# Performance work log

Hardware: AMD Instinct MI355X
Metric: run time of the kernel (lower is better)

The kernel has to match this reference:

```python
import jax, jax.numpy as jnp
import numpy as np

GROUPS = 1  # module-level groups arg


def adaptive_avg_pool(x, out_size):
    # Equal-tile average pool (exact match to torch AdaptiveAvgPool2d when H,W divisible by out_size)
    b, c, h, w = x.shape
    fh, fw = h // out_size, w // out_size
    return x.reshape(b, c, out_size, fh, out_size, fw).mean(axis=(3, 5))


def setup_inputs() -> dict:
    key = jax.random.key(0)
    k1, k2, k3, k4 = jax.random.split(key, 4)
    x = jax.random.normal(k1, (64, 128, 80, 80), jnp.float32)
    weight = jax.random.normal(k2, (128, 128, 3, 3), jnp.float32) * 0.05   # static conv weight [out, icg, k, k]
    w_att = jax.random.normal(k3, (16384, 1, 3, 3), jnp.float32) * 0.05    # conv_att weight (groups=icg=128)
    b_att = jax.random.normal(k4, (16384,), jnp.float32) * 0.05            # conv_att bias
    return {"x": x, "weight": weight, "w_att": w_att, "b_att": b_att}


def reference(x, weight, w_att, b_att):
    b, cin, h, w = x.shape
    out_ch, icg, k, _ = weight.shape  # icg = in_channels // groups
    pad = 1

    # attention branch: adaptive avg pool to (k+2), grouped 3x3 VALID conv -> [b, out*icg, k, k]
    avg = adaptive_avg_pool(x, k + 2)
    att = jax.lax.conv_general_dilated(avg, w_att, (1, 1), "VALID",
                                       feature_group_count=icg)
    att = jax.nn.sigmoid(att + b_att[None, :, None, None])
    att = att.reshape(b, out_ch, icg, k, k)

    # per-sample dynamic kernels
    dyn_w = weight[None] * att                    # [b, out, icg, k, k]

    # batch-grouped conv: fold batch into channels, groups = b * GROUPS
    xg = x.reshape(1, b * cin, h, w)
    wg = dyn_w.reshape(b * out_ch, icg, k, k)
    out = jax.lax.conv_general_dilated(xg, wg, (1, 1), [(pad, pad), (pad, pad)],
                                       feature_group_count=b * GROUPS)
    return out.reshape(b, out_ch, out.shape[-2], out.shape[-1])
```

## Files before the change

### kernel.cpp

```cpp
#include <hip/hip_runtime.h>

typedef __bf16 bf16;
typedef __bf16 bf16x8 __attribute__((ext_vector_type(8)));
typedef float f32x16 __attribute__((ext_vector_type(16)));

#define NB 64
#define NC 128
#define HW 80

#define XT_BYTES  110166016L
#define W2_BYTES  18874368L
#define AVG_BYTES 819200L
#define WS_NEEDED (XT_BYTES + W2_BYTES + AVG_BYTES)

__device__ __forceinline__ void async16(const void* g, void* l) {
    __builtin_amdgcn_global_load_lds((const __attribute__((address_space(1))) void*)g,
                                     (__attribute__((address_space(3))) void*)l, 16, 0, 0);
}

__global__ void zero_halo(bf16* __restrict__ xT) {
    int b = blockIdx.x;
    long base = (long)b * 82 * 82 * 128;
    uint4 z = make_uint4(0u, 0u, 0u, 0u);
    for (int k = threadIdx.x; k < 5184; k += 256) {
        long off;
        if (k < 1312) {
            off = (long)k * 8;
        } else if (k < 2624) {
            off = (long)81 * 82 * 128 + (long)(k - 1312) * 8;
        } else {
            int r = k - 2624;
            int Y = (r >> 5) + 1;
            int side = (r >> 4) & 1;
            int cq = r & 15;
            off = ((long)Y * 82 + side * 81) * 128 + cq * 8;
        }
        *reinterpret_cast<uint4*>(xT + base + off) = z;
    }
}

__global__ void transpose_kernel(const float* __restrict__ x, bf16* __restrict__ xT) {
    __shared__ __align__(16) bf16 tile[64 * 68];
    int b = blockIdx.z, icb = blockIdx.y, pxb = blockIdx.x;
    int t = threadIdx.x;
    int pl = t & 63;
    int ig = t >> 6;
    const float* src = x + ((long)(b * 128 + icb * 64) * 6400) + pxb * 64;
    #pragma unroll
    for (int it = 0; it < 16; ++it) {
        int ic = ig * 16 + it;
        float v = src[(long)ic * 6400 + pl];
        tile[pl * 68 + ic] = (bf16)v;
    }
    __syncthreads();
    #pragma unroll
    for (int it = 0; it < 4; ++it) {
        int idx = it * 256 + t;
        int pxl = idx >> 4;
        int icq = idx & 15;
        int px = pxb * 64 + pxl;
        int Y = px / 80 + 1, X = px % 80 + 1;
        uint2 v = *reinterpret_cast<const uint2*>(&tile[pxl * 68 + icq * 4]);
        *reinterpret_cast<uint2*>(&xT[(((long)b * 82 + Y) * 82 + X) * 128 + icb * 64 + icq * 4]) = v;
    }
}

__global__ void pool_kernel(const bf16* __restrict__ xT, float* __restrict__ avg) {
    __shared__ float part[256][8];
    int bid = blockIdx.x;
    int j = bid % 5; int t2 = bid / 5; int i = t2 % 5; int b = t2 / 5;
    int t = threadIdx.x;
    int pxg = t >> 4, cc = t & 15;
    const bf16* src = xT + (((long)b * 82 + 1 + i * 16) * 82 + 1 + j * 16 + pxg) * 128 + cc * 8;
    float s[8];
    #pragma unroll
    for (int e = 0; e < 8; ++e) s[e] = 0.f;
    #pragma unroll
    for (int dy = 0; dy < 16; ++dy) {
        bf16x8 v = *reinterpret_cast<const bf16x8*>(src + (long)dy * 82 * 128);
        #pragma unroll
        for (int e = 0; e < 8; ++e) s[e] += (float)v[e];
    }
    #pragma unroll
    for (int e = 0; e < 8; ++e) part[t][e] = s[e];
    __syncthreads();
    if (t < 128) {
        int cc2 = t >> 3, e = t & 7;
        float sum = 0.f;
        #pragma unroll
        for (int g = 0; g < 16; ++g) sum += part[g * 16 + cc2][e];
        avg[(((long)b * 128 + cc2 * 8 + e) * 5 + i) * 5 + j] = sum * (1.0f / 256.0f);
    }
}

__global__ void att_kernel(const float* __restrict__ avg, const float* __restrict__ weight,
                           const float* __restrict__ w_att, const float* __restrict__ b_att,
                           bf16* __restrict__ W2) {
    __shared__ float sa[25];
    int b = blockIdx.x >> 7, och = blockIdx.x & 127;
    int ic = threadIdx.x;
    if (ic < 25) sa[ic] = avg[(long)blockIdx.x * 25 + ic];
    __syncthreads();
    int o = och * 128 + ic;
    float wa[9];
    #pragma unroll
    for (int j = 0; j < 9; ++j) wa[j] = w_att[(long)o * 9 + j];
    float bias = b_att[o];
    const float* wst = weight + (long)o * 9;
    #pragma unroll
    for (int kh = 0; kh < 3; ++kh) {
        #pragma unroll
        for (int kw = 0; kw < 3; ++kw) {
            float z = bias;
            #pragma unroll
            for (int di = 0; di < 3; ++di)
                #pragma unroll
                for (int dj = 0; dj < 3; ++dj)
                    z += sa[(kh + di) * 5 + (kw + dj)] * wa[di * 3 + dj];
            float s = 1.0f / (1.0f + __expf(-z));
            float dw = wst[kh * 3 + kw] * s;
            int p = kh * 3 + kw;
            W2[(((long)b * 9 + p) * 128 + och) * 128 + ic] = (bf16)dw;
        }
    }
}

__global__ __launch_bounds__(256, 2)
void conv_gemm(const bf16* __restrict__ xT, const bf16* __restrict__ W2,
               float* __restrict__ out) {
    __shared__ __align__(16) bf16 Xs[180 * 128];
    __shared__ __align__(16) bf16 Ws[2][128 * 64];
    int b = blockIdx.z;
    int px0 = blockIdx.x * 16;
    int py0 = blockIdx.y * 8;
    int t = threadIdx.x;
    int wave = t >> 6, lane = t & 63;
    int l31 = lane & 31, hl = lane >> 5;
    int ow = (wave >> 1) * 64;
    int nw = (wave & 1) * 64;

    {
        const bf16* xsrc = xT + (((long)b * 82 + py0) * 82 + px0) * 128;
        for (int cidx = wave; cidx < 45; cidx += 4) {
            int idx0 = cidx << 6;
            int idx = idx0 + lane;
            int pf = idx >> 4, icb = idx & 15;
            int r = pf / 18, cx = pf - r * 18;
            async16(xsrc + ((long)r * 82 + cx) * 128 + ((icb ^ (pf & 7)) << 3),
                    &Xs[idx0 * 8]);
        }
        const bf16* wsrc = W2 + (long)b * 9 * 16384;
        #pragma unroll
        for (int it = 0; it < 4; ++it) {
            int idx0 = it * 256 + (wave << 6);
            int idx = idx0 + lane;
            int och = idx >> 3, icb = idx & 7;
            async16(wsrc + och * 128 + ((icb ^ (och & 7)) << 3), &Ws[0][idx0 * 8]);
        }
    }
    asm volatile("s_waitcnt vmcnt(0)" ::: "memory");
    __builtin_amdgcn_s_barrier();
    asm volatile("" ::: "memory");

    f32x16 acc[2][2];
    #pragma unroll
    for (int mi = 0; mi < 2; ++mi)
        #pragma unroll
        for (int ni = 0; ni < 2; ++ni)
            #pragma unroll
            for (int r = 0; r < 16; ++r) acc[mi][ni][r] = 0.f;

    int aRow0 = (ow + l31) * 64;
    int sA = l31 & 7;
    int pfb = ((nw + l31) >> 4) * 18 + ((nw + l31) & 15);

    #pragma unroll
    for (int tt = 0; tt < 18; ++tt) {
        int p = tt >> 1, h = tt & 1;
        int kh = p / 3, kw = p - kh * 3;
        if (tt < 17) {
            int p2 = (tt + 1) >> 1, h2 = (tt + 1) & 1;
            const bf16* wsrc = W2 + ((long)b * 9 + p2) * 16384 + h2 * 64;
            bf16* ldst = &Ws[(tt + 1) & 1][0];
            #pragma unroll
            for (int it = 0; it < 4; ++it) {
                int idx0 = it * 256 + (wave << 6);
                int idx = idx0 + lane;
                int och = idx >> 3, icb = idx & 7;
                async16(wsrc + och * 128 + ((icb ^ (och & 7)) << 3), ldst + idx0 * 8);
            }
        }
        const bf16* Wb = &Ws[tt & 1][0];
        __builtin_amdgcn_s_setprio(1);
        #pragma unroll
        for (int ks = 0; ks < 4; ++ks) {
            int icb = ks * 2 + hl;
            bf16x8 a0 = *reinterpret_cast<const bf16x8*>(Wb + aRow0 + ((icb ^ sA) << 3));
            bf16x8 a1 = *reinterpret_cast<const bf16x8*>(Wb + aRow0 + 2048 + ((icb ^ sA) << 3));
            int icbx = h * 8 + icb;
            int pf0 = pfb + kh * 18 + kw;
            int pf1 = pf0 + 36;
            bf16x8 b0 = *reinterpret_cast<const bf16x8*>(&Xs[pf0 * 128 + ((icbx ^ (pf0 & 7)) << 3)]);
            bf16x8 b1 = *reinterpret_cast<const bf16x8*>(&Xs[pf1 * 128 + ((icbx ^ (pf1 & 7)) << 3)]);
            acc[0][0] = __builtin_amdgcn_mfma_f32_32x32x16_bf16(a0, b0, acc[0][0], 0, 0, 0);
            acc[0][1] = __builtin_amdgcn_mfma_f32_32x32x16_bf16(a0, b1, acc[0][1], 0, 0, 0);
            acc[1][0] = __builtin_amdgcn_mfma_f32_32x32x16_bf16(a1, b0, acc[1][0], 0, 0, 0);
            acc[1][1] = __builtin_amdgcn_mfma_f32_32x32x16_bf16(a1, b1, acc[1][1], 0, 0, 0);
        }
        __builtin_amdgcn_s_setprio(0);
        __builtin_amdgcn_sched_barrier(0);
        asm volatile("s_waitcnt vmcnt(0)" ::: "memory");
        __builtin_amdgcn_s_barrier();
        asm volatile("" ::: "memory");
    }

    #pragma unroll
    for (int mi = 0; mi < 2; ++mi) {
        #pragma unroll
        for (int ni = 0; ni < 2; ++ni) {
            int n = nw + ni * 32 + l31;
            int oy = py0 + (n >> 4), ox = px0 + (n & 15);
            float* ob = out + ((long)(b * 128 + ow + mi * 32 + 4 * hl) * 80 + oy) * 80 + ox;
            #pragma unroll
            for (int reg = 0; reg < 16; ++reg) {
                int row = (reg & 3) + 8 * (reg >> 2);
                ob[(long)row * 6400] = acc[mi][ni][reg];
            }
        }
    }
}

extern "C" void kernel_launch(void* const* d_in, const int* in_sizes, int n_in,
                              void* d_out, int out_size, void* d_ws, size_t ws_size,
                              hipStream_t stream) {
    const float* x      = (const float*)d_in[0];
    const float* weight = (const float*)d_in[1];
    const float* w_att  = (const float*)d_in[2];
    const float* b_att  = (const float*)d_in[3];
    float* out = (float*)d_out;

    if (ws_size < (size_t)WS_NEEDED) return;

    char* ws = (char*)d_ws;
    bf16* xT  = (bf16*)ws;
    bf16* W2  = (bf16*)(ws + XT_BYTES);
    float* avg = (float*)(ws + XT_BYTES + W2_BYTES);

    zero_halo<<<64, 256, 0, stream>>>(xT);
    transpose_kernel<<<dim3(100, 2, 64), 256, 0, stream>>>(x, xT);
    pool_kernel<<<1600, 256, 0, stream>>>(xT, avg);
    att_kernel<<<8192, 128, 0, stream>>>(avg, weight, w_att, b_att, W2);
    conv_gemm<<<dim3(5, 10, 64), 256, 0, stream>>>(xT, W2, out);
}
```

Before: 521.5 us.

## Fuse pool+attention, merge halo zeroing, read conv weights directly from global

Folds halo zeroing into the transpose kernel and merges pooling and attention into one kernel, reducing launches and the avg round-trip. The dynamic weights are written in an MFMA-fragment-friendly layout so the conv kernel loads A operands straight from global memory instead of double-buffering them through LDS with per-step barriers. This frees LDS so occupancy can rise to 3 blocks per CU. The trade-off is exposed global load latency in the MFMA loop and a low-parallelism pool_att kernel with serialized barriers.

```diff
diff --git a/kernel.cpp b/kernel.cpp
--- a/kernel.cpp
+++ b/kernel.cpp
@@ -1,48 +1,47 @@
 #include <hip/hip_runtime.h>
 
 typedef __bf16 bf16;
+typedef __bf16 bf16x2 __attribute__((ext_vector_type(2)));
 typedef __bf16 bf16x8 __attribute__((ext_vector_type(8)));
 typedef float f32x16 __attribute__((ext_vector_type(16)));
 
-#define NB 64
-#define NC 128
-#define HW 80
-
 #define XT_BYTES  110166016L
 #define W2_BYTES  18874368L
-#define AVG_BYTES 819200L
-#define WS_NEEDED (XT_BYTES + W2_BYTES + AVG_BYTES)
+#define WS_NEEDED (XT_BYTES + W2_BYTES)
 
 __device__ __forceinline__ void async16(const void* g, void* l) {
     __builtin_amdgcn_global_load_lds((const __attribute__((address_space(1))) void*)g,
                                      (__attribute__((address_space(3))) void*)l, 16, 0, 0);
-}
-
-__global__ void zero_halo(bf16* __restrict__ xT) {
-    int b = blockIdx.x;
-    long base = (long)b * 82 * 82 * 128;
-    uint4 z = make_uint4(0u, 0u, 0u, 0u);
-    for (int k = threadIdx.x; k < 5184; k += 256) {
-        long off;
-        if (k < 1312) {
-            off = (long)k * 8;
-        } else if (k < 2624) {
-            off = (long)81 * 82 * 128 + (long)(k - 1312) * 8;
-        } else {
-            int r = k - 2624;
-            int Y = (r >> 5) + 1;
-            int side = (r >> 4) & 1;
-            int cq = r & 15;
-            off = ((long)Y * 82 + side * 81) * 128 + cq * 8;
-        }
-        *reinterpret_cast<uint4*>(xT + base + off) = z;
-    }
 }
 
 __global__ void transpose_kernel(const float* __restrict__ x, bf16* __restrict__ xT) {
     __shared__ __align__(16) bf16 tile[64 * 68];
     int b = blockIdx.z, icb = blockIdx.y, pxb = blockIdx.x;
     int t = threadIdx.x;
+
+    {
+        int bid2 = blockIdx.y * 100 + blockIdx.x;
+        if (t < 26) {
+            int k = bid2 * 26 + t;
+            if (k < 5184) {
+                long off;
+                if (k < 1312) {
+                    off = (long)k * 8;
+                } else if (k < 2624) {
+                    off = (long)81 * 82 * 128 + (long)(k - 1312) * 8;
+                } else {
+                    int r = k - 2624;
+                    int Y = (r >> 5) + 1;
+                    int side = (r >> 4) & 1;
+                    int cq = r & 15;
+                    off = ((long)Y * 82 + side * 81) * 128 + cq * 8;
+                }
+                *reinterpret_cast<uint4*>(xT + (long)b * 82 * 82 * 128 + off) =
+                    make_uint4(0u, 0u, 0u, 0u);
+            }
+        }
+    }
+
     int pl = t & 63;
     int ig = t >> 6;
     const float* src = x + ((long)(b * 128 + icb * 64) * 6400) + pxb * 64;
@@ -65,71 +64,74 @@
     }
 }
 
-__global__ void pool_kernel(const bf16* __restrict__ xT, float* __restrict__ avg) {
-    __shared__ float part[256][8];
-    int bid = blockIdx.x;
-    int j = bid % 5; int t2 = bid / 5; int i = t2 % 5; int b = t2 / 5;
+__global__ void pool_att(const bf16* __restrict__ xT, const float* __restrict__ weight,
+                         const float* __restrict__ w_att, const float* __restrict__ b_att,
+                         bf16* __restrict__ W2k) {
+    __shared__ float part[16][16][2];
+    __shared__ float avgs[32][25];
+    int b = blockIdx.x >> 2, cg = blockIdx.x & 3;
     int t = threadIdx.x;
-    int pxg = t >> 4, cc = t & 15;
-    const bf16* src = xT + (((long)b * 82 + 1 + i * 16) * 82 + 1 + j * 16 + pxg) * 128 + cc * 8;
-    float s[8];
-    #pragma unroll
-    for (int e = 0; e < 8; ++e) s[e] = 0.f;
-    #pragma unroll
-    for (int dy = 0; dy < 16; ++dy) {
-        bf16x8 v = *reinterpret_cast<const bf16x8*>(src + (long)dy * 82 * 128);
-        #pragma unroll
-        for (int e = 0; e < 8; ++e) s[e] += (float)v[e];
-    }
-    #pragma unroll
-    for (int e = 0; e < 8; ++e) part[t][e] = s[e];
-    __syncthreads();
-    if (t < 128) {
-        int cc2 = t >> 3, e = t & 7;
-        float sum = 0.f;
-        #pragma unroll
-        for (int g = 0; g < 16; ++g) sum += part[g * 16 + cc2][e];
-        avg[(((long)b * 128 + cc2 * 8 + e) * 5 + i) * 5 + j] = sum * (1.0f / 256.0f);
-    }
-}
-
-__global__ void att_kernel(const float* __restrict__ avg, const float* __restrict__ weight,
-                           const float* __restrict__ w_att, const float* __restrict__ b_att,
-                           bf16* __restrict__ W2) {
-    __shared__ float sa[25];
-    int b = blockIdx.x >> 7, och = blockIdx.x & 127;
-    int ic = threadIdx.x;
-    if (ic < 25) sa[ic] = avg[(long)blockIdx.x * 25 + ic];
-    __syncthreads();
-    int o = och * 128 + ic;
-    float wa[9];
-    #pragma unroll
-    for (int j = 0; j < 9; ++j) wa[j] = w_att[(long)o * 9 + j];
-    float bias = b_att[o];
-    const float* wst = weight + (long)o * 9;
-    #pragma unroll
-    for (int kh = 0; kh < 3; ++kh) {
-        #pragma unroll
-        for (int kw = 0; kw < 3; ++kw) {
-            float z = bias;
-            #pragma unroll
-            for (int di = 0; di < 3; ++di)
+    int pg = t >> 4, ch2 = t & 15;
+
+    for (int ij = 0; ij < 25; ++ij) {
+        int i = ij / 5, j = ij - i * 5;
+        const bf16* src = xT + (((long)b * 82 + 1 + i * 16 + pg) * 82 + 1 + j * 16) * 128
+                          + cg * 32 + ch2 * 2;
+        float s0 = 0.f, s1 = 0.f;
+        #pragma unroll
+        for (int dx = 0; dx < 16; ++dx) {
+            bf16x2 v = *reinterpret_cast<const bf16x2*>(src + dx * 128);
+            s0 += (float)v[0];
+            s1 += (float)v[1];
+        }
+        part[pg][ch2][0] = s0;
+        part[pg][ch2][1] = s1;
+        __syncthreads();
+        if (t < 32) {
+            int cr = t >> 1, half = t & 1;
+            float s = 0.f;
+            #pragma unroll
+            for (int g = 0; g < 16; ++g) s += part[g][cr][half];
+            avgs[cr * 2 + half][ij] = s * (1.0f / 256.0f);
+        }
+        __syncthreads();
+    }
+
+    int ic = t & 127, ochl = t >> 7;
+    #pragma unroll 2
+    for (int ol = 0; ol < 16; ++ol) {
+        int ochL = ochl * 16 + ol;
+        int ochG = cg * 32 + ochL;
+        long o = (long)ochG * 128 + ic;
+        float wa[9];
+        #pragma unroll
+        for (int jj = 0; jj < 9; ++jj) wa[jj] = w_att[o * 9 + jj];
+        float bias = b_att[o];
+        const float* wst = weight + o * 9;
+        const float* sa = &avgs[ochL][0];
+        #pragma unroll
+        for (int kh = 0; kh < 3; ++kh) {
+            #pragma unroll
+            for (int kw = 0; kw < 3; ++kw) {
+                float z = bias;
                 #pragma unroll
-                for (int dj = 0; dj < 3; ++dj)
-                    z += sa[(kh + di) * 5 + (kw + dj)] * wa[di * 3 + dj];
-            float s = 1.0f / (1.0f + __expf(-z));
-            float dw = wst[kh * 3 + kw] * s;
-            int p = kh * 3 + kw;
-            W2[(((long)b * 9 + p) * 128 + och) * 128 + ic] = (bf16)dw;
-        }
-    }
-}
-
-__global__ __launch_bounds__(256, 2)
-void conv_gemm(const bf16* __restrict__ xT, const bf16* __restrict__ W2,
+                for (int di = 0; di < 3; ++di)
+                    #pragma unroll
+                    for (int dj = 0; dj < 3; ++dj)
+                        z += sa[(kh + di) * 5 + (kw + dj)] * wa[di * 3 + dj];
+                float s = 1.0f / (1.0f + __expf(-z));
+                float dw = wst[kh * 3 + kw] * s;
+                int p = kh * 3 + kw;
+                W2k[((((long)b * 9 + p) * 16 + (ic >> 3)) * 128 + ochG) * 8 + (ic & 7)] = (bf16)dw;
+            }
+        }
+    }
+}
+
+__global__ __launch_bounds__(256, 3)
+void conv_gemm(const bf16* __restrict__ xT, const bf16* __restrict__ W2k,
                float* __restrict__ out) {
     __shared__ __align__(16) bf16 Xs[180 * 128];
-    __shared__ __align__(16) bf16 Ws[2][128 * 64];
     int b = blockIdx.z;
     int px0 = blockIdx.x * 16;
     int py0 = blockIdx.y * 8;
@@ -149,14 +151,6 @@
             async16(xsrc + ((long)r * 82 + cx) * 128 + ((icb ^ (pf & 7)) << 3),
                     &Xs[idx0 * 8]);
         }
-        const bf16* wsrc = W2 + (long)b * 9 * 16384;
-        #pragma unroll
-        for (int it = 0; it < 4; ++it) {
-            int idx0 = it * 256 + (wave << 6);
-            int idx = idx0 + lane;
-            int och = idx >> 3, icb = idx & 7;
-            async16(wsrc + och * 128 + ((icb ^ (och & 7)) << 3), &Ws[0][idx0 * 8]);
-        }
     }
     asm volatile("s_waitcnt vmcnt(0)" ::: "memory");
     __builtin_amdgcn_s_barrier();
@@ -170,48 +164,32 @@
             #pragma unroll
             for (int r = 0; r < 16; ++r) acc[mi][ni][r] = 0.f;
 
-    int aRow0 = (ow + l31) * 64;
-    int sA = l31 & 7;
     int pfb = ((nw + l31) >> 4) * 18 + ((nw + l31) & 15);
-
-    #pragma unroll
-    for (int tt = 0; tt < 18; ++tt) {
-        int p = tt >> 1, h = tt & 1;
-        int kh = p / 3, kw = p - kh * 3;
-        if (tt < 17) {
-            int p2 = (tt + 1) >> 1, h2 = (tt + 1) & 1;
-            const bf16* wsrc = W2 + ((long)b * 9 + p2) * 16384 + h2 * 64;
-            bf16* ldst = &Ws[(tt + 1) & 1][0];
-            #pragma unroll
-            for (int it = 0; it < 4; ++it) {
-                int idx0 = it * 256 + (wave << 6);
-                int idx = idx0 + lane;
-                int och = idx >> 3, icb = idx & 7;
-                async16(wsrc + och * 128 + ((icb ^ (och & 7)) << 3), ldst + idx0 * 8);
-            }
-        }
-        const bf16* Wb = &Ws[tt & 1][0];
+    const bf16* Ab = W2k + (long)b * 9 * 16384 + hl * 1024 + (ow + l31) * 8;
+
+    for (int p = 0; p < 9; ++p) {
+        int kh = (p >= 6) ? 2 : ((p >= 3) ? 1 : 0);
+        int kw = p - kh * 3;
+        int pf0 = pfb + kh * 18 + kw;
+        int pf1 = pf0 + 36;
+        const bf16* Ap = Ab + (long)p * 16384;
+        const bf16* B0 = &Xs[pf0 * 128];
+        const bf16* B1 = &Xs[pf1 * 128];
+        int s0 = pf0 & 7, s1 = pf1 & 7;
         __builtin_amdgcn_s_setprio(1);
         #pragma unroll
-        for (int ks = 0; ks < 4; ++ks) {
-            int icb = ks * 2 + hl;
-            bf16x8 a0 = *reinterpret_cast<const bf16x8*>(Wb + aRow0 + ((icb ^ sA) << 3));
-            bf16x8 a1 = *reinterpret_cast<const bf16x8*>(Wb + aRow0 + 2048 + ((icb ^ sA) << 3));
-            int icbx = h * 8 + icb;
-            int pf0 = pfb + kh * 18 + kw;
-            int pf1 = pf0 + 36;
-            bf16x8 b0 = *reinterpret_cast<const bf16x8*>(&Xs[pf0 * 128 + ((icbx ^ (pf0 & 7)) << 3)]);
-            bf16x8 b1 = *reinterpret_cast<const bf16x8*>(&Xs[pf1 * 128 + ((icbx ^ (pf1 & 7)) << 3)]);
+        for (int ks = 0; ks < 8; ++ks) {
+            int kc = ks * 2 + hl;
+            bf16x8 a0 = *reinterpret_cast<const bf16x8*>(Ap + ks * 2048);
+            bf16x8 a1 = *reinterpret_cast<const bf16x8*>(Ap + ks * 2048 + 256);
+            bf16x8 b0 = *reinterpret_cast<const bf16x8*>(B0 + ((kc ^ s0) << 3));
+            bf16x8 b1 = *reinterpret_cast<const bf16x8*>(B1 + ((kc ^ s1) << 3));
             acc[0][0] = __builtin_amdgcn_mfma_f32_32x32x16_bf16(a0, b0, acc[0][0], 0, 0, 0);
             acc[0][1] = __builtin_amdgcn_mfma_f32_32x32x16_bf16(a0, b1, acc[0][1], 0, 0, 0);
             acc[1][0] = __builtin_amdgcn_mfma_f32_32x32x16_bf16(a1, b0, acc[1][0], 0, 0, 0);
             acc[1][1] = __builtin_amdgcn_mfma_f32_32x32x16_bf16(a1, b1, acc[1][1], 0, 0, 0);
         }
         __builtin_amdgcn_s_setprio(0);
-        __builtin_amdgcn_sched_barrier(0);
-        asm volatile("s_waitcnt vmcnt(0)" ::: "memory");
-        __builtin_amdgcn_s_barrier();
-        asm volatile("" ::: "memory");
     }
 
     #pragma unroll
@@ -243,12 +221,9 @@
 
     char* ws = (char*)d_ws;
     bf16* xT  = (bf16*)ws;
-    bf16* W2  = (bf16*)(ws + XT_BYTES);
-    float* avg = (float*)(ws + XT_BYTES + W2_BYTES);
-
-    zero_halo<<<64, 256, 0, stream>>>(xT);
+    bf16* W2k = (bf16*)(ws + XT_BYTES);
+
     transpose_kernel<<<dim3(100, 2, 64), 256, 0, stream>>>(x, xT);
-    pool_kernel<<<1600, 256, 0, stream>>>(xT, avg);
-    att_kernel<<<8192, 128, 0, stream>>>(avg, weight, w_att, b_att, W2);
-    conv_gemm<<<dim3(5, 10, 64), 256, 0, stream>>>(xT, W2, out);
-}
+    pool_att<<<256, 256, 0, stream>>>(xT, weight, w_att, b_att, W2k);
+    conv_gemm<<<dim3(5, 10, 64), 256, 0, stream>>>(xT, W2k, out);
+}
```

New measurement: 590.6 us. 13.2% more time.

## Load dynamic weights straight to registers, drop per-tap barriers, fuse halo zeroing

Applied to the files above, without the earlier changes.

The dynamic weights are stored in a fragment-friendly k-blocked layout so each wave loads its MFMA A operands straight from global memory into registers, double-buffered across the 9 kernel taps. This removes the LDS weight staging and the barrier plus vmcnt wait after every half-tap. Halo zeroing moves into the transpose kernel, saving a launch, and pool reads now walk contiguous pixels. The cost is 32 extra bf16x8 registers per thread, which may lower occupancy or spill, and each wave re-reads weights from L2 with no sharing through LDS.

```diff
diff --git a/kernel.cpp b/kernel.cpp
--- a/kernel.cpp
+++ b/kernel.cpp
@@ -3,10 +3,6 @@
 typedef __bf16 bf16;
 typedef __bf16 bf16x8 __attribute__((ext_vector_type(8)));
 typedef float f32x16 __attribute__((ext_vector_type(16)));
-
-#define NB 64
-#define NC 128
-#define HW 80
 
 #define XT_BYTES  110166016L
 #define W2_BYTES  18874368L
@@ -18,31 +14,34 @@
                                      (__attribute__((address_space(3))) void*)l, 16, 0, 0);
 }
 
-__global__ void zero_halo(bf16* __restrict__ xT) {
-    int b = blockIdx.x;
-    long base = (long)b * 82 * 82 * 128;
-    uint4 z = make_uint4(0u, 0u, 0u, 0u);
-    for (int k = threadIdx.x; k < 5184; k += 256) {
-        long off;
-        if (k < 1312) {
-            off = (long)k * 8;
-        } else if (k < 2624) {
-            off = (long)81 * 82 * 128 + (long)(k - 1312) * 8;
-        } else {
-            int r = k - 2624;
-            int Y = (r >> 5) + 1;
-            int side = (r >> 4) & 1;
-            int cq = r & 15;
-            off = ((long)Y * 82 + side * 81) * 128 + cq * 8;
-        }
-        *reinterpret_cast<uint4*>(xT + base + off) = z;
-    }
-}
-
 __global__ void transpose_kernel(const float* __restrict__ x, bf16* __restrict__ xT) {
     __shared__ __align__(16) bf16 tile[64 * 68];
     int b = blockIdx.z, icb = blockIdx.y, pxb = blockIdx.x;
     int t = threadIdx.x;
+
+    {
+        int bid2 = blockIdx.y * 100 + blockIdx.x;
+        if (t < 26) {
+            int k = bid2 * 26 + t;
+            if (k < 5184) {
+                long off;
+                if (k < 1312) {
+                    off = (long)k * 8;
+                } else if (k < 2624) {
+                    off = (long)81 * 82 * 128 + (long)(k - 1312) * 8;
+                } else {
+                    int r = k - 2624;
+                    int Y = (r >> 5) + 1;
+                    int side = (r >> 4) & 1;
+                    int cq = r & 15;
+                    off = ((long)Y * 82 + side * 81) * 128 + cq * 8;
+                }
+                *reinterpret_cast<uint4*>(xT + (long)b * 82 * 82 * 128 + off) =
+                    make_uint4(0u, 0u, 0u, 0u);
+            }
+        }
+    }
+
     int pl = t & 63;
     int ig = t >> 6;
     const float* src = x + ((long)(b * 128 + icb * 64) * 6400) + pxb * 64;
@@ -71,13 +70,13 @@
     int j = bid % 5; int t2 = bid / 5; int i = t2 % 5; int b = t2 / 5;
     int t = threadIdx.x;
     int pxg = t >> 4, cc = t & 15;
-    const bf16* src = xT + (((long)b * 82 + 1 + i * 16) * 82 + 1 + j * 16 + pxg) * 128 + cc * 8;
+    const bf16* src = xT + (((long)b * 82 + 1 + i * 16 + pxg) * 82 + 1 + j * 16) * 128 + cc * 8;
     float s[8];
     #pragma unroll
     for (int e = 0; e < 8; ++e) s[e] = 0.f;
     #pragma unroll
     for (int dy = 0; dy < 16; ++dy) {
-        bf16x8 v = *reinterpret_cast<const bf16x8*>(src + (long)dy * 82 * 128);
+        bf16x8 v = *reinterpret_cast<const bf16x8*>(src + (long)dy * 128);
         #pragma unroll
         for (int e = 0; e < 8; ++e) s[e] += (float)v[e];
     }
@@ -95,7 +94,7 @@
 
 __global__ void att_kernel(const float* __restrict__ avg, const float* __restrict__ weight,
                            const float* __restrict__ w_att, const float* __restrict__ b_att,
-                           bf16* __restrict__ W2) {
+                           bf16* __restrict__ W2k) {
     __shared__ float sa[25];
     int b = blockIdx.x >> 7, och = blockIdx.x & 127;
     int ic = threadIdx.x;
@@ -120,16 +119,15 @@
             float s = 1.0f / (1.0f + __expf(-z));
             float dw = wst[kh * 3 + kw] * s;
             int p = kh * 3 + kw;
-            W2[(((long)b * 9 + p) * 128 + och) * 128 + ic] = (bf16)dw;
+            W2k[((((long)b * 9 + p) * 16 + (ic >> 3)) * 128 + och) * 8 + (ic & 7)] = (bf16)dw;
         }
     }
 }
 
 __global__ __launch_bounds__(256, 2)
-void conv_gemm(const bf16* __restrict__ xT, const bf16* __restrict__ W2,
+void conv_gemm(const bf16* __restrict__ xT, const bf16* __restrict__ W2k,
                float* __restrict__ out) {
     __shared__ __align__(16) bf16 Xs[180 * 128];
-    __shared__ __align__(16) bf16 Ws[2][128 * 64];
     int b = blockIdx.z;
     int px0 = blockIdx.x * 16;
     int py0 = blockIdx.y * 8;
@@ -138,6 +136,15 @@
     int l31 = lane & 31, hl = lane >> 5;
     int ow = (wave >> 1) * 64;
     int nw = (wave & 1) * 64;
+
+    const bf16* Ab = W2k + (long)b * 9 * 16384 + hl * 1024 + (ow + l31) * 8;
+
+    bf16x8 Abuf[2][16];
+    #pragma unroll
+    for (int ks = 0; ks < 8; ++ks) {
+        Abuf[0][ks * 2]     = *reinterpret_cast<const bf16x8*>(Ab + ks * 2048);
+        Abuf[0][ks * 2 + 1] = *reinterpret_cast<const bf16x8*>(Ab + ks * 2048 + 256);
+    }
 
     {
         const bf16* xsrc = xT + (((long)b * 82 + py0) * 82 + px0) * 128;
@@ -149,14 +156,6 @@
             async16(xsrc + ((long)r * 82 + cx) * 128 + ((icb ^ (pf & 7)) << 3),
                     &Xs[idx0 * 8]);
         }
-        const bf16* wsrc = W2 + (long)b * 9 * 16384;
-        #pragma unroll
-        for (int it = 0; it < 4; ++it) {
-            int idx0 = it * 256 + (wave << 6);
-            int idx = idx0 + lane;
-            int och = idx >> 3, icb = idx & 7;
-            async16(wsrc + och * 128 + ((icb ^ (och & 7)) << 3), &Ws[0][idx0 * 8]);
-        }
     }
     asm volatile("s_waitcnt vmcnt(0)" ::: "memory");
     __builtin_amdgcn_s_barrier();
@@ -170,48 +169,37 @@
             #pragma unroll
             for (int r = 0; r < 16; ++r) acc[mi][ni][r] = 0.f;
 
-    int aRow0 = (ow + l31) * 64;
-    int sA = l31 & 7;
     int pfb = ((nw + l31) >> 4) * 18 + ((nw + l31) & 15);
 
     #pragma unroll
-    for (int tt = 0; tt < 18; ++tt) {
-        int p = tt >> 1, h = tt & 1;
-        int kh = p / 3, kw = p - kh * 3;
-        if (tt < 17) {
-            int p2 = (tt + 1) >> 1, h2 = (tt + 1) & 1;
-            const bf16* wsrc = W2 + ((long)b * 9 + p2) * 16384 + h2 * 64;
-            bf16* ldst = &Ws[(tt + 1) & 1][0];
-            #pragma unroll
-            for (int it = 0; it < 4; ++it) {
-                int idx0 = it * 256 + (wave << 6);
-                int idx = idx0 + lane;
-                int och = idx >> 3, icb = idx & 7;
-                async16(wsrc + och * 128 + ((icb ^ (och & 7)) << 3), ldst + idx0 * 8);
+    for (int p = 0; p < 9; ++p) {
+        const int cur = p & 1, nxt = cur ^ 1;
+        if (p < 8) {
+            const bf16* Ap = Ab + (long)(p + 1) * 16384;
+            #pragma unroll
+            for (int ks = 0; ks < 8; ++ks) {
+                Abuf[nxt][ks * 2]     = *reinterpret_cast<const bf16x8*>(Ap + ks * 2048);
+                Abuf[nxt][ks * 2 + 1] = *reinterpret_cast<const bf16x8*>(Ap + ks * 2048 + 256);
             }
         }
-        const bf16* Wb = &Ws[tt & 1][0];
+        const int kh = p / 3, kw = p - kh * 3;
+        int pf0 = pfb + kh * 18 + kw;
+        int pf1 = pf0 + 36;
+        const bf16* B0 = &Xs[pf0 * 128];
+        const bf16* B1 = &Xs[pf1 * 128];
+        int s0 = pf0 & 7, s1 = pf1 & 7;
         __builtin_amdgcn_s_setprio(1);
         #pragma unroll
-        for (int ks = 0; ks < 4; ++ks) {
-            int icb = ks * 2 + hl;
-            bf16x8 a0 = *reinterpret_cast<const bf16x8*>(Wb + aRow0 + ((icb ^ sA) << 3));
-            bf16x8 a1 = *reinterpret_cast<const bf16x8*>(Wb + aRow0 + 2048 + ((icb ^ sA) << 3));
-            int icbx = h * 8 + icb;
-            int pf0 = pfb + kh * 18 + kw;
-            int pf1 = pf0 + 36;
-            bf16x8 b0 = *reinterpret_cast<const bf16x8*>(&Xs[pf0 * 128 + ((icbx ^ (pf0 & 7)) << 3)]);
-            bf16x8 b1 = *reinterpret_cast<const bf16x8*>(&Xs[pf1 * 128 + ((icbx ^ (pf1 & 7)) << 3)]);
-            acc[0][0] = __builtin_amdgcn_mfma_f32_32x32x16_bf16(a0, b0, acc[0][0], 0, 0, 0);
-            acc[0][1] = __builtin_amdgcn_mfma_f32_32x32x16_bf16(a0, b1, acc[0][1], 0, 0, 0);
-            acc[1][0] = __builtin_amdgcn_mfma_f32_32x32x16_bf16(a1, b0, acc[1][0], 0, 0, 0);
-            acc[1][1] = __builtin_amdgcn_mfma_f32_32x32x16_bf16(a1, b1, acc[1][1], 0, 0, 0);
+        for (int ks = 0; ks < 8; ++ks) {
+            int kc = ks * 2 + hl;
+            bf16x8 b0 = *reinterpret_cast<const bf16x8*>(B0 + ((kc ^ s0) << 3));
+            bf16x8 b1 = *reinterpret_cast<const bf16x8*>(B1 + ((kc ^ s1) << 3));
+            acc[0][0] = __builtin_amdgcn_mfma_f32_32x32x16_bf16(Abuf[cur][ks * 2],     b0, acc[0][0], 0, 0, 0);
+            acc[0][1] = __builtin_amdgcn_mfma_f32_32x32x16_bf16(Abuf[cur][ks * 2],     b1, acc[0][1], 0, 0, 0);
+            acc[1][0] = __builtin_amdgcn_mfma_f32_32x32x16_bf16(Abuf[cur][ks * 2 + 1], b0, acc[1][0], 0, 0, 0);
+            acc[1][1] = __builtin_amdgcn_mfma_f32_32x32x16_bf16(Abuf[cur][ks * 2 + 1], b1, acc[1][1], 0, 0, 0);
         }
         __builtin_amdgcn_s_setprio(0);
-        __builtin_amdgcn_sched_barrier(0);
-        asm volatile("s_waitcnt vmcnt(0)" ::: "memory");
-        __builtin_amdgcn_s_barrier();
-        asm volatile("" ::: "memory");
     }
 
     #pragma unroll
@@ -243,12 +231,11 @@
 
     char* ws = (char*)d_ws;
     bf16* xT  = (bf16*)ws;
-    bf16* W2  = (bf16*)(ws + XT_BYTES);
+    bf16* W2k = (bf16*)(ws + XT_BYTES);
     float* avg = (float*)(ws + XT_BYTES + W2_BYTES);
 
-    zero_halo<<<64, 256, 0, stream>>>(xT);
     transpose_kernel<<<dim3(100, 2, 64), 256, 0, stream>>>(x, xT);
     pool_kernel<<<1600, 256, 0, stream>>>(xT, avg);
-    att_kernel<<<8192, 128, 0, stream>>>(avg, weight, w_att, b_att, W2);
-    conv_gemm<<<dim3(5, 10, 64), 256, 0, stream>>>(xT, W2, out);
-}
+    att_kernel<<<8192, 128, 0, stream>>>(avg, weight, w_att, b_att, W2k);
+    conv_gemm<<<dim3(5, 10, 64), 256, 0, stream>>>(xT, W2k, out);
+}
```

Result: faster. 503.4 us (-3.5%).
